# Kernel optimization log

Hardware: AMD Instinct MI355X
Metric: run time of the kernel (lower is better)

The kernel has to match this reference:

```python
import jax, jax.numpy as jnp
import numpy as np

D_MODEL = 2048
H_TOTAL = 32
D_HEAD = D_MODEL // H_TOTAL  # 64
H_ACTIVE = 4
ROPE_BASE = 10000.0


def _apply_rope(t, cos, sin):
    # t: [B, H, T, DH]; cos/sin: [T, DH//2]; interleaved pair rotation
    t1 = t[..., 0::2]
    t2 = t[..., 1::2]
    r1 = t1 * cos - t2 * sin
    r2 = t1 * sin + t2 * cos
    return jnp.stack([r1, r2], axis=-1).reshape(t.shape)


def setup_inputs() -> dict:
    key = jax.random.key(0)
    ks = jax.random.split(key, 4)
    x = jax.random.normal(ks[0], (4, 1024, D_MODEL), dtype=jnp.float32)
    w_router = jax.random.normal(ks[1], (D_MODEL, H_TOTAL), dtype=jnp.float32) * 0.02
    w_qkv = jax.random.normal(ks[2], (D_MODEL, 3 * D_MODEL), dtype=jnp.float32) * 0.02
    w_out = jax.random.normal(ks[3], (D_MODEL, D_MODEL), dtype=jnp.float32) * 0.02
    return {"x": x, "w_router": w_router, "w_qkv": w_qkv, "w_out": w_out}


def reference(x, w_router, w_qkv, w_out):
    B, T, _ = x.shape
    # --- SwitchRouter: per-token probabilities over heads ---
    probs = jax.nn.softmax(x @ w_router, axis=-1)            # [B, T, H]
    # top-h_active heads per token (dense-math equivalent of sparse dispatch)
    _, top_idx = jax.lax.top_k(probs, H_ACTIVE)              # [B, T, HA]
    mask = jnp.sum(jax.nn.one_hot(top_idx, H_TOTAL, dtype=x.dtype), axis=-2)  # [B, T, H]
    gate = probs * mask                                      # router-scored gate

    # --- QKV projection ---
    qkv = x @ w_qkv                                          # [B, T, 3D]
    q, k, v = jnp.split(qkv, 3, axis=-1)
    def to_heads(t):
        return t.reshape(B, T, H_TOTAL, D_HEAD).transpose(0, 2, 1, 3)  # [B, H, T, DH]
    q, k, v = to_heads(q), to_heads(k), to_heads(v)

    # --- RoPE ---
    inv_freq = 1.0 / (ROPE_BASE ** (jnp.arange(0, D_HEAD, 2, dtype=jnp.float32) / D_HEAD))
    ang = jnp.arange(T, dtype=jnp.float32)[:, None] * inv_freq[None, :]  # [T, DH/2]
    cos, sin = jnp.cos(ang), jnp.sin(ang)
    q = _apply_rope(q, cos, sin)
    k = _apply_rope(k, cos, sin)

    # --- causal SDPA ---
    scores = jnp.einsum('bhqd,bhkd->bhqk', q, k) / np.float32(np.sqrt(D_HEAD))
    causal = jnp.tril(jnp.ones((T, T), dtype=bool))
    scores = jnp.where(causal, scores, jnp.finfo(scores.dtype).min)
    attn = jax.nn.softmax(scores, axis=-1)
    out = jnp.einsum('bhqk,bhkd->bhqd', attn, v)             # [B, H, T, DH]

    # --- gate: only active heads contribute (scatter-back equivalent) ---
    out = out * gate.transpose(0, 2, 1)[..., None]           # [B, H, T, DH]
    out = out.transpose(0, 2, 1, 3).reshape(B, T, D_MODEL)
    return out @ w_out
```

## Files before the change

kernel.cpp:

```cpp
#include <hip/hip_runtime.h>
#include <hip/hip_bf16.h>
#include <stdint.h>
#include <stddef.h>

typedef __attribute__((ext_vector_type(8))) short bf16x8;
typedef __attribute__((ext_vector_type(8))) unsigned short u16x8;
typedef __attribute__((ext_vector_type(4))) float f32x4;
typedef __attribute__((ext_vector_type(16))) float f32x16;

#define TT 1024

__device__ __forceinline__ unsigned short f2bf(float f){
  unsigned u = __builtin_bit_cast(unsigned, f);
  unsigned r = 0x7fffu + ((u >> 16) & 1u);
  return (unsigned short)((u + r) >> 16);
}
__device__ __forceinline__ float bf2f(unsigned short s){
  unsigned u = ((unsigned)s) << 16;
  return __builtin_bit_cast(float, u);
}
__device__ __forceinline__ void gload16(const unsigned short* g, unsigned short* l){
  __builtin_amdgcn_global_load_lds(
      (const __attribute__((address_space(1))) void*)g,
      (__attribute__((address_space(3))) void*)l, 16, 0, 0);
}

#define MFMA32(a, b, c) __builtin_amdgcn_mfma_f32_32x32x16_bf16((a), (b), (c), 0, 0, 0)
#define MFMA_B16(a, b, c) __builtin_amdgcn_mfma_f32_16x16x32_bf16((a), (b), (c), 0, 0, 0)

__global__ void transpose_w_kernel(const float* __restrict__ wqkv, const float* __restrict__ wout,
                                   unsigned short* __restrict__ wqkvT, unsigned short* __restrict__ woutT){
  __shared__ float tile[32][33];
  const float* in; unsigned short* out; int C;
  int bx = blockIdx.x;
  if (bx < 192){ in = wqkv; out = wqkvT; C = 6144; }
  else         { in = wout; out = woutT; C = 2048; bx -= 192; }
  const int R = 2048;
  int c0 = bx * 32, r0 = blockIdx.y * 32;
  for (int i = threadIdx.y; i < 32; i += 8)
    tile[i][threadIdx.x] = in[(size_t)(r0 + i) * C + c0 + threadIdx.x];
  __syncthreads();
  for (int i = threadIdx.y; i < 32; i += 8)
    out[(size_t)(c0 + i) * R + r0 + threadIdx.x] = f2bf(tile[threadIdx.x][i]);
}

__global__ __launch_bounds__(256) void prep_kernel(const float* __restrict__ x,
                                                   const float* __restrict__ wr,
                                                   unsigned short* __restrict__ x_bf,
                                                   float* __restrict__ gate,
                                                   unsigned char* __restrict__ heads4,
                                                   float* __restrict__ tab){
  __shared__ float xc[8 * 256];
  __shared__ float red[8 * 8 * 32];
  const int tid = threadIdx.x;
  const int tok0 = blockIdx.x * 8;
  const int p = tid >> 5, h = tid & 31;

  if (blockIdx.x < 128){
    int i2 = blockIdx.x * 256 + tid;
    int pos = i2 >> 5, ii = i2 & 31;
    float freq = powf(10000.0f, -(float)ii / 32.0f);
    float ang = (float)pos * freq;
    tab[i2 * 2]     = cosf(ang);
    tab[i2 * 2 + 1] = sinf(ang);
  }

  float acc[8] = {0.f,0.f,0.f,0.f,0.f,0.f,0.f,0.f};
  for (int kb = 0; kb < 8; kb++){
    __syncthreads();
    {
      int tok = tid >> 5, e = (tid & 31) * 8;
      const float* xp = x + (size_t)(tok0 + tok) * 2048 + kb * 256 + e;
      float4 v0 = *(const float4*)xp, v1 = *(const float4*)(xp + 4);
      float vals[8] = {v0.x, v0.y, v0.z, v0.w, v1.x, v1.y, v1.z, v1.w};
      u16x8 ob;
      #pragma unroll
      for (int jj = 0; jj < 8; jj++) ob[jj] = f2bf(vals[jj]);
      *(u16x8*)(x_bf + (size_t)(tok0 + tok) * 2048 + kb * 256 + e) = ob;
      #pragma unroll
      for (int jj = 0; jj < 8; jj++) xc[tok * 256 + e + jj] = vals[jj];
    }
    __syncthreads();
    const float* wp = wr + (size_t)(kb * 256 + p * 32) * 32 + h;
    #pragma unroll 4
    for (int j = 0; j < 32; j++){
      float wv = wp[j * 32];
      #pragma unroll
      for (int tok = 0; tok < 8; tok++)
        acc[tok] += xc[tok * 256 + p * 32 + j] * wv;
    }
  }
  #pragma unroll
  for (int tok = 0; tok < 8; tok++) red[(p * 8 + tok) * 32 + h] = acc[tok];
  __syncthreads();
  {
    int lane = tid & 63;
    int tok = (tid >> 6) * 2 + (lane >> 5);
    int hh = lane & 31;
    float logit = 0.f;
    #pragma unroll
    for (int pp = 0; pp < 8; pp++) logit += red[(pp * 8 + tok) * 32 + hh];
    float m = logit;
    #pragma unroll
    for (int s = 16; s >= 1; s >>= 1) m = fmaxf(m, __shfl_xor(m, s));
    float e = __expf(logit - m);
    float sum = e;
    #pragma unroll
    for (int s = 16; s >= 1; s >>= 1) sum += __shfl_xor(sum, s);
    float prob = e / sum;
    float v = logit; int sel = 0;
    #pragma unroll
    for (int rr2 = 0; rr2 < 4; rr2++){
      float bv = v; int bi = hh;
      #pragma unroll
      for (int s = 16; s >= 1; s >>= 1){
        float ov = __shfl_xor(bv, s); int oi = __shfl_xor(bi, s);
        if (ov > bv || (ov == bv && oi < bi)) { bv = ov; bi = oi; }
      }
      if (hh == bi) { sel = 1; v = -3.4e38f; }
    }
    gate[(size_t)(tok0 + tok) * 32 + hh] = sel ? prob : 0.f;
    unsigned long long bal = __ballot(sel != 0);
    unsigned selmask = (unsigned)(bal >> ((lane >> 5) * 32));
    if (sel){
      int r = __popc(selmask & ((1u << hh) - 1u));
      heads4[(size_t)(tok0 + tok) * 4 + r] = (unsigned char)hh;
    }
  }
}

__global__ void compact_kernel(const unsigned char* __restrict__ heads4,
                               unsigned short* __restrict__ idx, int* __restrict__ counts){
  int bh = blockIdx.x;
  int b = bh >> 5, h = bh & 31;
  int lane = threadIdx.x;
  int base = 0;
  for (int c = 0; c < 16; c++){
    int t = c * 64 + lane;
    unsigned u = ((const unsigned*)heads4)[b * 1024 + t];
    int r = -1;
    if (((u      ) & 255) == (unsigned)h) r = 0;
    else if (((u >>  8) & 255) == (unsigned)h) r = 1;
    else if (((u >> 16) & 255) == (unsigned)h) r = 2;
    else if (((u >> 24) & 255) == (unsigned)h) r = 3;
    bool act = (r >= 0);
    unsigned long long mask = __ballot(act);
    int pos = base + __popcll(mask & ((1ull << lane) - 1ull));
    if (act) idx[bh * 1024 + pos] = (unsigned short)(t | (r << 10));
    base += __popcll(mask);
  }
  if (lane == 0) counts[bh] = base;
}

__global__ __launch_bounds__(256) void qgemm_kernel(const unsigned short* __restrict__ x_bf,
                                                    const unsigned short* __restrict__ wqkvT,
                                                    const unsigned short* __restrict__ idx,
                                                    const int* __restrict__ counts,
                                                    const float* __restrict__ tab,
                                                    unsigned short* __restrict__ qact){
  __shared__ float red[4][64][64];
  const int bh = blockIdx.x, qt = blockIdx.y;
  const int count = counts[bh];
  if (qt * 64 >= count) return;
  const int b = bh >> 5, h = bh & 31;
  const int tid = threadIdx.x, lane = tid & 63, w = tid >> 6;
  const int li = lane & 15, lg = lane >> 4;
  const int nvalid = min(64, count - qt * 64);
  const unsigned short* myidx = idx + bh * 1024 + qt * 64;

  int atok[4];
  #pragma unroll
  for (int ai = 0; ai < 4; ai++){
    int s = ai * 16 + li;
    atok[ai] = (s < nvalid) ? (myidx[s] & 1023) : 0;
  }
  const unsigned short* Bbase = wqkvT + (size_t)(h * 64) * 2048;

  f32x4 acc[4][4];
  #pragma unroll
  for (int i = 0; i < 4; i++)
    #pragma unroll
    for (int j = 0; j < 4; j++) acc[i][j] = f32x4{0.f, 0.f, 0.f, 0.f};

  const int k0w = w * 512;
  #pragma unroll 2
  for (int ks = 0; ks < 16; ks++){
    int k0 = k0w + ks * 32 + lg * 8;
    bf16x8 af[4], bw[4];
    #pragma unroll
    for (int ai = 0; ai < 4; ai++)
      af[ai] = *(const bf16x8*)(x_bf + (size_t)(b * 1024 + atok[ai]) * 2048 + k0);
    #pragma unroll
    for (int ni = 0; ni < 4; ni++)
      bw[ni] = *(const bf16x8*)(Bbase + (size_t)(ni * 16 + li) * 2048 + k0);
    #pragma unroll
    for (int ai = 0; ai < 4; ai++)
      #pragma unroll
      for (int ni = 0; ni < 4; ni++)
        acc[ai][ni] = MFMA_B16(af[ai], bw[ni], acc[ai][ni]);
  }
  #pragma unroll
  for (int ai = 0; ai < 4; ai++)
    #pragma unroll
    for (int ni = 0; ni < 4; ni++)
      #pragma unroll
      for (int rr = 0; rr < 4; rr++)
        red[w][ai * 16 + lg * 4 + rr][ni * 16 + li] = acc[ai][ni][rr];
  __syncthreads();

  int q = tid >> 2, dbase = (tid & 3) * 16;
  if (q < nvalid){
    int e = myidx[q];
    int tok = e & 1023, r = e >> 10;
    unsigned short* op = qact + ((size_t)((b << 10) + tok) * 4 + r) * 64;
    const float* tp = tab + ((size_t)tok * 32 + (dbase >> 1)) * 2;
    #pragma unroll
    for (int p = 0; p < 8; p++){
      int d0 = dbase + 2 * p;
      float v0 = red[0][q][d0] + red[1][q][d0] + red[2][q][d0] + red[3][q][d0];
      float v1 = red[0][q][d0 + 1] + red[1][q][d0 + 1] + red[2][q][d0 + 1] + red[3][q][d0 + 1];
      float c = tp[2 * p], s = tp[2 * p + 1];
      op[d0]     = f2bf(v0 * c - v1 * s);
      op[d0 + 1] = f2bf(v0 * s + v1 * c);
    }
  }
}

__global__ __launch_bounds__(256, 2) void gemmk(const unsigned short* __restrict__ A,
                                                const unsigned short* __restrict__ Bt,
                                                unsigned short* __restrict__ kbuf,
                                                unsigned short* __restrict__ vt,
                                                const float* __restrict__ tab,
                                                int K, int nbm){
  extern __shared__ unsigned short smem[];
  constexpr int MREP = 4;
  constexpr int BM = MREP * 64;
  constexpr int AU = MREP * 2048;
  constexpr int SLOT = AU + 4096;
  const int nblk = gridDim.x;
  const int raw = blockIdx.x;
  const int tile = (raw & 7) * (nblk >> 3) + (raw >> 3);
  const int bn = tile / nbm, bm = tile % nbm;

  const int tid = threadIdx.x, lane = tid & 63, wid = tid >> 6;
  const int wrow = wid >> 1, wcol = wid & 1;
  const int l31 = lane & 31, hi = lane >> 5;
  const int X = ((l31 >> 1) & 7) << 4;

  const unsigned short* gA[MREP];
  const unsigned short* gB[2];
  #pragma unroll
  for (int p = 0; p < MREP; p++){
    int L = tid * 16 + p * 4096;
    int line = L >> 7;
    int cs = (L & 127) ^ ((line & 7) << 4);
    gA[p] = A + (size_t)(bm * BM + line * 2 + (cs >> 6)) * K + ((cs & 63) >> 1);
  }
  #pragma unroll
  for (int p = 0; p < 2; p++){
    int L = tid * 16 + p * 4096;
    int line = L >> 7;
    int cs = (L & 127) ^ ((line & 7) << 4);
    gB[p] = Bt + (size_t)(bn * 128 + line * 2 + (cs >> 6)) * K + ((cs & 63) >> 1);
  }

  f32x16 acc[MREP][2];
  #pragma unroll
  for (int i = 0; i < MREP; i++)
    #pragma unroll
    for (int j = 0; j < 2; j++) acc[i][j] = f32x16{0,0,0,0,0,0,0,0,0,0,0,0,0,0,0,0};

  const int NT = K >> 5;
  #pragma unroll
  for (int tt = 0; tt < 2; tt++){
    unsigned short* sb = smem + tt * SLOT;
    #pragma unroll
    for (int p = 0; p < MREP; p++) gload16(gA[p] + (size_t)tt * 32, sb + tid * 8 + p * 2048);
    #pragma unroll
    for (int p = 0; p < 2; p++)    gload16(gB[p] + (size_t)tt * 32, sb + AU + tid * 8 + p * 2048);
  }

  for (int t = 0; t < NT; ++t){
    if (t < NT - 1) asm volatile("s_waitcnt vmcnt(6)" ::: "memory");
    else            asm volatile("s_waitcnt vmcnt(0)" ::: "memory");
    __builtin_amdgcn_s_barrier();
    __builtin_amdgcn_sched_barrier(0);
    const unsigned short* bs = smem + (t % 3) * SLOT;
    unsigned short* ns = smem + ((t + 2) % 3) * SLOT;
    const bool st = (t + 2 < NT);
    #pragma unroll
    for (int ks = 0; ks < 2; ks++){
      const int bo = (((l31 & 1) * 64 + ks * 32 + hi * 16) ^ X) >> 1;
      bf16x8 av[MREP], bv[2];
      #pragma unroll
      for (int i = 0; i < MREP; i++)
        av[i] = *(const bf16x8*)(bs + (wrow * (MREP * 16) + i * 16 + (l31 >> 1)) * 64 + bo);
      #pragma unroll
      for (int j = 0; j < 2; j++)
        bv[j] = *(const bf16x8*)(bs + AU + (wcol * 32 + j * 16 + (l31 >> 1)) * 64 + bo);
      if (st){
        if (ks == 0){
          #pragma unroll
          for (int p = 0; p < 3; p++)
            gload16(gA[p] + (size_t)(t + 2) * 32, ns + tid * 8 + p * 2048);
        } else {
          gload16(gA[3] + (size_t)(t + 2) * 32, ns + tid * 8 + 3 * 2048);
          #pragma unroll
          for (int p = 0; p < 2; p++)
            gload16(gB[p] + (size_t)(t + 2) * 32, ns + AU + tid * 8 + p * 2048);
        }
      }
      #pragma unroll
      for (int i = 0; i < MREP; i++){
        acc[i][0] = MFMA32(av[i], bv[0], acc[i][0]);
        acc[i][1] = MFMA32(av[i], bv[1], acc[i][1]);
      }
    }
  }

  if (bn < 16){
    #pragma unroll
    for (int i = 0; i < MREP; i++){
      #pragma unroll
      for (int j = 0; j < 2; j++){
        int col = bn * 128 + wcol * 64 + j * 32 + l31;
        int ii = (col & 63) >> 1;
        #pragma unroll
        for (int g = 0; g < 4; g++){
          #pragma unroll
          for (int rr = 0; rr < 4; rr++){
            int row = bm * BM + wrow * (BM / 2) + i * 32 + g * 8 + hi * 4 + rr;
            int pos = row & (TT - 1);
            const float* tp = tab + ((size_t)pos * 32 + ii) * 2;
            float c = tp[0], s = tp[1];
            float val = acc[i][j][g * 4 + rr];
            float pv = __shfl_xor(val, 1);
            float res = (lane & 1) ? (pv * s + val * c) : (val * c - pv * s);
            kbuf[(size_t)row * 2048 + col] = f2bf(res);
          }
        }
      }
    }
  } else {
    #pragma unroll
    for (int i = 0; i < MREP; i++){
      #pragma unroll
      for (int j = 0; j < 2; j++){
        int vcol = bn * 128 + wcol * 64 + j * 32 + l31 - 2048;
        int hh = vcol >> 6, d = vcol & 63;
        int row0 = bm * BM + wrow * (BM / 2) + i * 32 + hi * 4;
        int b = row0 >> 10, t0 = row0 & (TT - 1);
        #pragma unroll
        for (int g = 0; g < 4; g++){
          ushort4 pk;
          pk.x = f2bf(acc[i][j][g * 4 + 0]); pk.y = f2bf(acc[i][j][g * 4 + 1]);
          pk.z = f2bf(acc[i][j][g * 4 + 2]); pk.w = f2bf(acc[i][j][g * 4 + 3]);
          *(ushort4*)(vt + ((size_t)((b * 32 + hh) * 64 + d)) * TT + t0 + g * 8) = pk;
        }
      }
    }
  }
}

__global__ __launch_bounds__(256) void attn_sparse_kernel(unsigned short* __restrict__ qact,
                                                          const unsigned short* __restrict__ kbuf,
                                                          const unsigned short* __restrict__ vt,
                                                          const float* __restrict__ gate,
                                                          const unsigned short* __restrict__ idx,
                                                          const int* __restrict__ counts){
  __shared__ unsigned short Ks[64 * 64];
  __shared__ unsigned short Vs[64 * 64];
  __shared__ unsigned short Ps[4][16 * 64];
  const int bh = blockIdx.x, qt = blockIdx.y;
  const int count = counts[bh];
  if (qt * 64 >= count) return;
  const int b = bh >> 5, h = bh & 31;
  const int tid = threadIdx.x, lane = tid & 63, w = tid >> 6;
  const int li = lane & 15, lg = lane >> 4;
  const unsigned short* myidx = idx + bh * 1024 + qt * 64;
  const int nvalid = min(64, count - qt * 64);
  const int qmax = myidx[nvalid - 1] & 1023;

  int qi[4];
  #pragma unroll
  for (int r = 0; r < 4; r++){
    int s = w * 16 + lg * 4 + r;
    qi[r] = (s < nvalid) ? (myidx[s] & 1023) : -1;
  }
  bf16x8 qf0, qf1;
  {
    int s = w * 16 + li;
    int e2 = (s < nvalid) ? myidx[s] : 0;
    const unsigned short* qp = qact + ((size_t)((b << 10) + (e2 & 1023)) * 4 + (e2 >> 10)) * 64;
    qf0 = *(const bf16x8*)(qp + lg * 8);
    qf1 = *(const bf16x8*)(qp + 32 + lg * 8);
  }
  f32x4 o[4];
  #pragma unroll
  for (int i = 0; i < 4; i++) o[i] = f32x4{0.f, 0.f, 0.f, 0.f};
  float m_run[4], l_run[4];
  #pragma unroll
  for (int r = 0; r < 4; r++){ m_run[r] = -1e30f; l_run[r] = 0.f; }

  const int nkt = (qmax >> 6) + 1;
  for (int kt = 0; kt < nkt; kt++){
    const int kb = kt * 64;
    #pragma unroll
    for (int s2 = 0; s2 < 2; s2++){
      int s = s2 * 256 + tid;
      int r = s >> 3, c = (s & 7) * 8;
      gload16(kbuf + (size_t)(b * TT + kb + r) * 2048 + h * 64 + c, &Ks[s * 8]);
      gload16(vt + (size_t)(bh * 64 + r) * TT + kb + c, &Vs[s * 8]);
    }
    __syncthreads();

    f32x4 s4[4];
    #pragma unroll
    for (int ni = 0; ni < 4; ni++){
      bf16x8 k0 = *(const bf16x8*)(&Ks[(ni * 16 + li) * 64 + lg * 8]);
      bf16x8 k1 = *(const bf16x8*)(&Ks[(ni * 16 + li) * 64 + 32 + lg * 8]);
      f32x4 t = f32x4{0.f, 0.f, 0.f, 0.f};
      t = MFMA_B16(qf0, k0, t);
      t = MFMA_B16(qf1, k1, t);
      s4[ni] = t;
    }
    float mt[4];
    #pragma unroll
    for (int r = 0; r < 4; r++) mt[r] = -1e30f;
    #pragma unroll
    for (int ni = 0; ni < 4; ni++){
      int kidx = kb + ni * 16 + li;
      #pragma unroll
      for (int r = 0; r < 4; r++){
        float val = s4[ni][r] * 0.125f;
        val = (kidx <= qi[r]) ? val : -1e30f;
        s4[ni][r] = val;
        mt[r] = fmaxf(mt[r], val);
      }
    }
    #pragma unroll
    for (int r = 0; r < 4; r++){
      #pragma unroll
      for (int sh = 8; sh >= 1; sh >>= 1) mt[r] = fmaxf(mt[r], __shfl_xor(mt[r], sh));
      float mnew = fmaxf(m_run[r], mt[r]);
      float corr = __expf(m_run[r] - mnew);
      m_run[r] = mnew;
      l_run[r] *= corr;
      #pragma unroll
      for (int j = 0; j < 4; j++) o[j][r] *= corr;
    }
    float rs[4] = {0.f, 0.f, 0.f, 0.f};
    #pragma unroll
    for (int ni = 0; ni < 4; ni++)
      #pragma unroll
      for (int r = 0; r < 4; r++){
        float p = __expf(s4[ni][r] - m_run[r]);
        s4[ni][r] = p;
        rs[r] += p;
      }
    #pragma unroll
    for (int r = 0; r < 4; r++){
      #pragma unroll
      for (int sh = 8; sh >= 1; sh >>= 1) rs[r] += __shfl_xor(rs[r], sh);
      l_run[r] += rs[r];
    }
    #pragma unroll
    for (int ni = 0; ni < 4; ni++)
      #pragma unroll
      for (int r = 0; r < 4; r++)
        Ps[w][(lg * 4 + r) * 64 + ni * 16 + li] = f2bf(s4[ni][r]);
    #pragma unroll
    for (int ks = 0; ks < 2; ks++){
      bf16x8 pa = *(const bf16x8*)(&Ps[w][li * 64 + ks * 32 + lg * 8]);
      #pragma unroll
      for (int ni = 0; ni < 4; ni++){
        bf16x8 vb = *(const bf16x8*)(&Vs[(ni * 16 + li) * 64 + ks * 32 + lg * 8]);
        o[ni] = MFMA_B16(pa, vb, o[ni]);
      }
    }
    __syncthreads();
  }
  #pragma unroll
  for (int r = 0; r < 4; r++){
    if (qi[r] < 0) continue;
    float g = gate[(size_t)(b * TT + qi[r]) * 32 + h];
    float inv = g / l_run[r];
    int e = myidx[w * 16 + lg * 4 + r];
    unsigned short* op = qact + ((size_t)((b << 10) + (e & 1023)) * 4 + (e >> 10)) * 64;
    #pragma unroll
    for (int ni = 0; ni < 4; ni++)
      op[ni * 16 + li] = f2bf(o[ni][r] * inv);
  }
}

__global__ __launch_bounds__(256) void outsp_kernel(const unsigned short* __restrict__ qact,
                                                    const unsigned short* __restrict__ woutT,
                                                    const unsigned short* __restrict__ idx,
                                                    const int* __restrict__ counts,
                                                    unsigned short* __restrict__ p0,
                                                    unsigned short* __restrict__ p1,
                                                    unsigned short* __restrict__ p2,
                                                    unsigned short* __restrict__ p3){
  __shared__ unsigned short As[64 * 64];
  __shared__ unsigned short sidx[64];
  const int bh = blockIdx.x, qt = blockIdx.y;
  const int count = counts[bh];
  if (qt * 64 >= count) return;
  const int b = bh >> 5, h = bh & 31;
  const int tid = threadIdx.x, lane = tid & 63, w = tid >> 6;
  const int li = lane & 15, lg = lane >> 4;
  const int nvalid = min(64, count - qt * 64);
  const unsigned short* myidx = idx + bh * 1024 + qt * 64;
  const int n0 = blockIdx.z * 256 + w * 64;

  bf16x8 bfr[4][2];
  #pragma unroll
  for (int ni = 0; ni < 4; ni++)
    #pragma unroll
    for (int kh = 0; kh < 2; kh++)
      bfr[ni][kh] = *(const bf16x8*)(woutT + (size_t)(n0 + ni * 16 + li) * 2048 + h * 64 + kh * 32 + lg * 8);

  if (tid < 64) sidx[tid] = myidx[(tid < nvalid) ? tid : 0];
  #pragma unroll
  for (int s2 = 0; s2 < 2; s2++){
    int s = s2 * 256 + tid;
    int row = s >> 3, bc = (s & 7) * 16;
    int e = myidx[(row < nvalid) ? row : 0];
    const unsigned short* src = qact + ((size_t)((b << 10) + (e & 1023)) * 4 + (e >> 10)) * 64;
    gload16(src + ((bc ^ ((row & 7) << 4)) >> 1), &As[s * 8]);
  }
  __syncthreads();

  const int kX = (li & 7) << 4;
  f32x4 acc[4][4];
  #pragma unroll
  for (int i = 0; i < 4; i++)
    #pragma unroll
    for (int j = 0; j < 4; j++) acc[i][j] = f32x4{0.f, 0.f, 0.f, 0.f};
  #pragma unroll
  for (int ti = 0; ti < 4; ti++){
    bf16x8 a0 = *(const bf16x8*)(&As[((ti * 16 + li) * 128 + ((lg * 16) ^ kX)) >> 1]);
    bf16x8 a1 = *(const bf16x8*)(&As[((ti * 16 + li) * 128 + ((64 + lg * 16) ^ kX)) >> 1]);
    #pragma unroll
    for (int ni = 0; ni < 4; ni++){
      acc[ti][ni] = MFMA_B16(a0, bfr[ni][0], acc[ti][ni]);
      acc[ti][ni] = MFMA_B16(a1, bfr[ni][1], acc[ti][ni]);
    }
  }
  #pragma unroll
  for (int ti = 0; ti < 4; ti++){
    #pragma unroll
    for (int rr = 0; rr < 4; rr++){
      int slot = ti * 16 + lg * 4 + rr;
      if (slot < nvalid){
        int e = sidx[slot];
        int tok = e & 1023, rk = e >> 10;
        unsigned short* pp = (rk == 0) ? p0 : (rk == 1) ? p1 : (rk == 2) ? p2 : p3;
        size_t base = (size_t)(b * 1024 + tok) * 2048 + n0;
        #pragma unroll
        for (int ni = 0; ni < 4; ni++)
          pp[base + ni * 16 + li] = f2bf(acc[ti][ni][rr]);
      }
    }
  }
}

__global__ void reduce_kernel(const unsigned short* __restrict__ p0,
                              const unsigned short* __restrict__ p1,
                              const unsigned short* __restrict__ p2,
                              const unsigned short* __restrict__ p3,
                              float* __restrict__ out){
  size_t i = ((size_t)blockIdx.x * 256 + threadIdx.x) * 8;
  u16x8 a = *(const u16x8*)(p0 + i);
  u16x8 b = *(const u16x8*)(p1 + i);
  u16x8 c = *(const u16x8*)(p2 + i);
  u16x8 d = *(const u16x8*)(p3 + i);
  #pragma unroll
  for (int j = 0; j < 8; j++)
    out[i + j] = bf2f(a[j]) + bf2f(b[j]) + bf2f(c[j]) + bf2f(d[j]);
}

extern "C" void kernel_launch(void* const* d_in, const int* in_sizes, int n_in,
                              void* d_out, int out_size, void* d_ws, size_t ws_size,
                              hipStream_t stream){
  const float* x        = (const float*)d_in[0];
  const float* w_router = (const float*)d_in[1];
  const float* w_qkv    = (const float*)d_in[2];
  const float* w_out    = (const float*)d_in[3];
  float* out = (float*)d_out;
  char* ws = (char*)d_ws;

  unsigned short* kbuf   = (unsigned short*)(ws);
  unsigned short* vt     = (unsigned short*)(ws + 16777216);
  unsigned short* qact   = (unsigned short*)(ws + 33554432);
  unsigned short* idx    = (unsigned short*)(ws + 37748736);
  int* counts            = (int*)(ws + 38010880);
  unsigned char* heads4  = (unsigned char*)(ws + 38011392);
  unsigned short* x_bf   = (unsigned short*)(ws + 50331648);
  unsigned short* wqkvT  = (unsigned short*)(ws + 67108864);
  unsigned short* woutT  = (unsigned short*)(ws + 92274688);
  float* gate            = (float*)(ws + 100663296);
  float* tab             = (float*)(ws + 101187584);
  unsigned short* part0  = kbuf;
  unsigned short* part1  = vt;
  unsigned short* part2  = x_bf;
  unsigned short* part3  = wqkvT;

  constexpr int KV_LDS = 3 * (4 * 4096 + 8192) * 2 / 2;
  (void)hipFuncSetAttribute(reinterpret_cast<const void*>(&gemmk),
                            hipFuncAttributeMaxDynamicSharedMemorySize, KV_LDS);

  hipLaunchKernelGGL(transpose_w_kernel, dim3(256, 64), dim3(32, 8), 0, stream, w_qkv, w_out, wqkvT, woutT);
  hipLaunchKernelGGL(prep_kernel, dim3(512), dim3(256), 0, stream, x, w_router, x_bf, gate, heads4, tab);
  hipLaunchKernelGGL(compact_kernel, dim3(128), dim3(64), 0, stream, heads4, idx, counts);
  hipLaunchKernelGGL(gemmk, dim3(512), dim3(256), KV_LDS, stream,
                     x_bf, wqkvT + (size_t)2048 * 2048, kbuf, vt, tab, 2048, 16);
  hipLaunchKernelGGL(qgemm_kernel, dim3(128, 16), dim3(256), 0, stream,
                     x_bf, wqkvT, idx, counts, tab, qact);
  hipLaunchKernelGGL(attn_sparse_kernel, dim3(128, 16), dim3(256), 0, stream,
                     qact, kbuf, vt, gate, idx, counts);
  hipLaunchKernelGGL(outsp_kernel, dim3(128, 16, 8), dim3(256), 0, stream,
                     qact, woutT, idx, counts, part0, part1, part2, part3);
  hipLaunchKernelGGL(reduce_kernel, dim3(4096), dim3(256), 0, stream,
                     part0, part1, part2, part3, out);
}
```

Baseline: 255.7 us.

## Merge weight transpose into prep and fuse K/V and Q GEMMs into one launch

```diff
diff --git a/kernel.cpp b/kernel.cpp
--- a/kernel.cpp
+++ b/kernel.cpp
@@ -28,31 +28,38 @@
 #define MFMA32(a, b, c) __builtin_amdgcn_mfma_f32_32x32x16_bf16((a), (b), (c), 0, 0, 0)
 #define MFMA_B16(a, b, c) __builtin_amdgcn_mfma_f32_16x16x32_bf16((a), (b), (c), 0, 0, 0)
 
-__global__ void transpose_w_kernel(const float* __restrict__ wqkv, const float* __restrict__ wout,
-                                   unsigned short* __restrict__ wqkvT, unsigned short* __restrict__ woutT){
-  __shared__ float tile[32][33];
-  const float* in; unsigned short* out; int C;
-  int bx = blockIdx.x;
-  if (bx < 192){ in = wqkv; out = wqkvT; C = 6144; }
-  else         { in = wout; out = woutT; C = 2048; bx -= 192; }
-  const int R = 2048;
-  int c0 = bx * 32, r0 = blockIdx.y * 32;
-  for (int i = threadIdx.y; i < 32; i += 8)
-    tile[i][threadIdx.x] = in[(size_t)(r0 + i) * C + c0 + threadIdx.x];
-  __syncthreads();
-  for (int i = threadIdx.y; i < 32; i += 8)
-    out[(size_t)(c0 + i) * R + r0 + threadIdx.x] = f2bf(tile[threadIdx.x][i]);
-}
-
-__global__ __launch_bounds__(256) void prep_kernel(const float* __restrict__ x,
-                                                   const float* __restrict__ wr,
-                                                   unsigned short* __restrict__ x_bf,
-                                                   float* __restrict__ gate,
-                                                   unsigned char* __restrict__ heads4,
-                                                   float* __restrict__ tab){
+__global__ __launch_bounds__(256) void prep2_kernel(const float* __restrict__ x,
+                                                    const float* __restrict__ wr,
+                                                    const float* __restrict__ wqkv,
+                                                    const float* __restrict__ wout,
+                                                    unsigned short* __restrict__ x_bf,
+                                                    float* __restrict__ gate,
+                                                    unsigned char* __restrict__ heads4,
+                                                    float* __restrict__ tab,
+                                                    unsigned short* __restrict__ wqkvT,
+                                                    unsigned short* __restrict__ woutT){
   __shared__ float xc[8 * 256];
   __shared__ float red[8 * 8 * 32];
+  __shared__ float tile[32][33];
   const int tid = threadIdx.x;
+
+  if (blockIdx.x >= 512){
+    int tb = blockIdx.x - 512;
+    int bx = tb & 255, by = tb >> 8;
+    const float* in; unsigned short* out; int C;
+    if (bx < 192){ in = wqkv; out = wqkvT; C = 6144; }
+    else         { in = wout; out = woutT; C = 2048; bx -= 192; }
+    const int R = 2048;
+    int c0 = bx * 32, r0 = by * 32;
+    int tx = tid & 31, ty = tid >> 5;
+    for (int i = ty; i < 32; i += 8)
+      tile[i][tx] = in[(size_t)(r0 + i) * C + c0 + tx];
+    __syncthreads();
+    for (int i = ty; i < 32; i += 8)
+      out[(size_t)(c0 + i) * R + r0 + tx] = f2bf(tile[tx][i]);
+    return;
+  }
+
   const int tok0 = blockIdx.x * 8;
   const int p = tid >> 5, h = tid & 31;
 
@@ -152,211 +159,220 @@
   if (lane == 0) counts[bh] = base;
 }
 
-__global__ __launch_bounds__(256) void qgemm_kernel(const unsigned short* __restrict__ x_bf,
-                                                    const unsigned short* __restrict__ wqkvT,
-                                                    const unsigned short* __restrict__ idx,
-                                                    const int* __restrict__ counts,
-                                                    const float* __restrict__ tab,
-                                                    unsigned short* __restrict__ qact){
-  __shared__ float red[4][64][64];
-  const int bh = blockIdx.x, qt = blockIdx.y;
-  const int count = counts[bh];
-  if (qt * 64 >= count) return;
-  const int b = bh >> 5, h = bh & 31;
-  const int tid = threadIdx.x, lane = tid & 63, w = tid >> 6;
-  const int li = lane & 15, lg = lane >> 4;
-  const int nvalid = min(64, count - qt * 64);
-  const unsigned short* myidx = idx + bh * 1024 + qt * 64;
-
-  int atok[4];
-  #pragma unroll
-  for (int ai = 0; ai < 4; ai++){
-    int s = ai * 16 + li;
-    atok[ai] = (s < nvalid) ? (myidx[s] & 1023) : 0;
-  }
-  const unsigned short* Bbase = wqkvT + (size_t)(h * 64) * 2048;
-
-  f32x4 acc[4][4];
-  #pragma unroll
-  for (int i = 0; i < 4; i++)
-    #pragma unroll
-    for (int j = 0; j < 4; j++) acc[i][j] = f32x4{0.f, 0.f, 0.f, 0.f};
-
-  const int k0w = w * 512;
-  #pragma unroll 2
-  for (int ks = 0; ks < 16; ks++){
-    int k0 = k0w + ks * 32 + lg * 8;
-    bf16x8 af[4], bw[4];
-    #pragma unroll
-    for (int ai = 0; ai < 4; ai++)
-      af[ai] = *(const bf16x8*)(x_bf + (size_t)(b * 1024 + atok[ai]) * 2048 + k0);
-    #pragma unroll
-    for (int ni = 0; ni < 4; ni++)
-      bw[ni] = *(const bf16x8*)(Bbase + (size_t)(ni * 16 + li) * 2048 + k0);
-    #pragma unroll
-    for (int ai = 0; ai < 4; ai++)
-      #pragma unroll
-      for (int ni = 0; ni < 4; ni++)
-        acc[ai][ni] = MFMA_B16(af[ai], bw[ni], acc[ai][ni]);
-  }
-  #pragma unroll
-  for (int ai = 0; ai < 4; ai++)
-    #pragma unroll
-    for (int ni = 0; ni < 4; ni++)
-      #pragma unroll
-      for (int rr = 0; rr < 4; rr++)
-        red[w][ai * 16 + lg * 4 + rr][ni * 16 + li] = acc[ai][ni][rr];
-  __syncthreads();
-
-  int q = tid >> 2, dbase = (tid & 3) * 16;
-  if (q < nvalid){
-    int e = myidx[q];
-    int tok = e & 1023, r = e >> 10;
-    unsigned short* op = qact + ((size_t)((b << 10) + tok) * 4 + r) * 64;
-    const float* tp = tab + ((size_t)tok * 32 + (dbase >> 1)) * 2;
-    #pragma unroll
-    for (int p = 0; p < 8; p++){
-      int d0 = dbase + 2 * p;
-      float v0 = red[0][q][d0] + red[1][q][d0] + red[2][q][d0] + red[3][q][d0];
-      float v1 = red[0][q][d0 + 1] + red[1][q][d0 + 1] + red[2][q][d0 + 1] + red[3][q][d0 + 1];
-      float c = tp[2 * p], s = tp[2 * p + 1];
-      op[d0]     = f2bf(v0 * c - v1 * s);
-      op[d0 + 1] = f2bf(v0 * s + v1 * c);
-    }
-  }
-}
-
-__global__ __launch_bounds__(256, 2) void gemmk(const unsigned short* __restrict__ A,
-                                                const unsigned short* __restrict__ Bt,
-                                                unsigned short* __restrict__ kbuf,
-                                                unsigned short* __restrict__ vt,
-                                                const float* __restrict__ tab,
-                                                int K, int nbm){
+__global__ __launch_bounds__(256, 2) void super_kernel(const unsigned short* __restrict__ x_bf,
+                                                       const unsigned short* __restrict__ wqkvT,
+                                                       unsigned short* __restrict__ kbuf,
+                                                       unsigned short* __restrict__ vt,
+                                                       const float* __restrict__ tab,
+                                                       const unsigned short* __restrict__ idx,
+                                                       const int* __restrict__ counts,
+                                                       unsigned short* __restrict__ qact){
   extern __shared__ unsigned short smem[];
-  constexpr int MREP = 4;
-  constexpr int BM = MREP * 64;
-  constexpr int AU = MREP * 2048;
-  constexpr int SLOT = AU + 4096;
-  const int nblk = gridDim.x;
-  const int raw = blockIdx.x;
-  const int tile = (raw & 7) * (nblk >> 3) + (raw >> 3);
-  const int bn = tile / nbm, bm = tile % nbm;
-
-  const int tid = threadIdx.x, lane = tid & 63, wid = tid >> 6;
-  const int wrow = wid >> 1, wcol = wid & 1;
-  const int l31 = lane & 31, hi = lane >> 5;
-  const int X = ((l31 >> 1) & 7) << 4;
-
-  const unsigned short* gA[MREP];
-  const unsigned short* gB[2];
-  #pragma unroll
-  for (int p = 0; p < MREP; p++){
-    int L = tid * 16 + p * 4096;
-    int line = L >> 7;
-    int cs = (L & 127) ^ ((line & 7) << 4);
-    gA[p] = A + (size_t)(bm * BM + line * 2 + (cs >> 6)) * K + ((cs & 63) >> 1);
-  }
-  #pragma unroll
-  for (int p = 0; p < 2; p++){
-    int L = tid * 16 + p * 4096;
-    int line = L >> 7;
-    int cs = (L & 127) ^ ((line & 7) << 4);
-    gB[p] = Bt + (size_t)(bn * 128 + line * 2 + (cs >> 6)) * K + ((cs & 63) >> 1);
-  }
-
-  f32x16 acc[MREP][2];
-  #pragma unroll
-  for (int i = 0; i < MREP; i++)
-    #pragma unroll
-    for (int j = 0; j < 2; j++) acc[i][j] = f32x16{0,0,0,0,0,0,0,0,0,0,0,0,0,0,0,0};
-
-  const int NT = K >> 5;
-  #pragma unroll
-  for (int tt = 0; tt < 2; tt++){
-    unsigned short* sb = smem + tt * SLOT;
-    #pragma unroll
-    for (int p = 0; p < MREP; p++) gload16(gA[p] + (size_t)tt * 32, sb + tid * 8 + p * 2048);
-    #pragma unroll
-    for (int p = 0; p < 2; p++)    gload16(gB[p] + (size_t)tt * 32, sb + AU + tid * 8 + p * 2048);
-  }
-
-  for (int t = 0; t < NT; ++t){
-    if (t < NT - 1) asm volatile("s_waitcnt vmcnt(6)" ::: "memory");
-    else            asm volatile("s_waitcnt vmcnt(0)" ::: "memory");
-    __builtin_amdgcn_s_barrier();
-    __builtin_amdgcn_sched_barrier(0);
-    const unsigned short* bs = smem + (t % 3) * SLOT;
-    unsigned short* ns = smem + ((t + 2) % 3) * SLOT;
-    const bool st = (t + 2 < NT);
-    #pragma unroll
-    for (int ks = 0; ks < 2; ks++){
-      const int bo = (((l31 & 1) * 64 + ks * 32 + hi * 16) ^ X) >> 1;
-      bf16x8 av[MREP], bv[2];
-      #pragma unroll
-      for (int i = 0; i < MREP; i++)
-        av[i] = *(const bf16x8*)(bs + (wrow * (MREP * 16) + i * 16 + (l31 >> 1)) * 64 + bo);
-      #pragma unroll
-      for (int j = 0; j < 2; j++)
-        bv[j] = *(const bf16x8*)(bs + AU + (wcol * 32 + j * 16 + (l31 >> 1)) * 64 + bo);
-      if (st){
-        if (ks == 0){
-          #pragma unroll
-          for (int p = 0; p < 3; p++)
-            gload16(gA[p] + (size_t)(t + 2) * 32, ns + tid * 8 + p * 2048);
-        } else {
-          gload16(gA[3] + (size_t)(t + 2) * 32, ns + tid * 8 + 3 * 2048);
-          #pragma unroll
-          for (int p = 0; p < 2; p++)
-            gload16(gB[p] + (size_t)(t + 2) * 32, ns + AU + tid * 8 + p * 2048);
-        }
-      }
-      #pragma unroll
-      for (int i = 0; i < MREP; i++){
-        acc[i][0] = MFMA32(av[i], bv[0], acc[i][0]);
-        acc[i][1] = MFMA32(av[i], bv[1], acc[i][1]);
-      }
-    }
-  }
-
-  if (bn < 16){
-    #pragma unroll
-    for (int i = 0; i < MREP; i++){
-      #pragma unroll
-      for (int j = 0; j < 2; j++){
-        int col = bn * 128 + wcol * 64 + j * 32 + l31;
-        int ii = (col & 63) >> 1;
-        #pragma unroll
-        for (int g = 0; g < 4; g++){
-          #pragma unroll
-          for (int rr = 0; rr < 4; rr++){
-            int row = bm * BM + wrow * (BM / 2) + i * 32 + g * 8 + hi * 4 + rr;
-            int pos = row & (TT - 1);
-            const float* tp = tab + ((size_t)pos * 32 + ii) * 2;
-            float c = tp[0], s = tp[1];
-            float val = acc[i][j][g * 4 + rr];
-            float pv = __shfl_xor(val, 1);
-            float res = (lane & 1) ? (pv * s + val * c) : (val * c - pv * s);
-            kbuf[(size_t)row * 2048 + col] = f2bf(res);
+  const int tid = threadIdx.x, lane = tid & 63;
+
+  if (blockIdx.x < 512){
+    const unsigned short* A  = x_bf;
+    const unsigned short* Bt = wqkvT + (size_t)2048 * 2048;
+    constexpr int MREP = 4;
+    constexpr int BM = 256;
+    constexpr int AU = MREP * 2048;
+    constexpr int SLOT = AU + 4096;
+    const int raw = blockIdx.x;
+    const int tile = (raw & 7) * 64 + (raw >> 3);
+    const int bn = tile >> 4, bm = tile & 15;
+    const int K = 2048;
+
+    const int wid = tid >> 6;
+    const int wrow = wid >> 1, wcol = wid & 1;
+    const int l31 = lane & 31, hi = lane >> 5;
+    const int X = ((l31 >> 1) & 7) << 4;
+
+    const unsigned short* gA[MREP];
+    const unsigned short* gB[2];
+    #pragma unroll
+    for (int p = 0; p < MREP; p++){
+      int L = tid * 16 + p * 4096;
+      int line = L >> 7;
+      int cs = (L & 127) ^ ((line & 7) << 4);
+      gA[p] = A + (size_t)(bm * BM + line * 2 + (cs >> 6)) * K + ((cs & 63) >> 1);
+    }
+    #pragma unroll
+    for (int p = 0; p < 2; p++){
+      int L = tid * 16 + p * 4096;
+      int line = L >> 7;
+      int cs = (L & 127) ^ ((line & 7) << 4);
+      gB[p] = Bt + (size_t)(bn * 128 + line * 2 + (cs >> 6)) * K + ((cs & 63) >> 1);
+    }
+
+    f32x16 acc[MREP][2];
+    #pragma unroll
+    for (int i = 0; i < MREP; i++)
+      #pragma unroll
+      for (int j = 0; j < 2; j++) acc[i][j] = f32x16{0,0,0,0,0,0,0,0,0,0,0,0,0,0,0,0};
+
+    const int NT = K >> 5;
+    #pragma unroll
+    for (int tt = 0; tt < 2; tt++){
+      unsigned short* sb = smem + tt * SLOT;
+      #pragma unroll
+      for (int p = 0; p < MREP; p++) gload16(gA[p] + (size_t)tt * 32, sb + tid * 8 + p * 2048);
+      #pragma unroll
+      for (int p = 0; p < 2; p++)    gload16(gB[p] + (size_t)tt * 32, sb + AU + tid * 8 + p * 2048);
+    }
+
+    for (int t = 0; t < NT; ++t){
+      if (t < NT - 1) asm volatile("s_waitcnt vmcnt(6)" ::: "memory");
+      else            asm volatile("s_waitcnt vmcnt(0)" ::: "memory");
+      __builtin_amdgcn_s_barrier();
+      __builtin_amdgcn_sched_barrier(0);
+      const unsigned short* bs = smem + (t % 3) * SLOT;
+      unsigned short* ns = smem + ((t + 2) % 3) * SLOT;
+      const bool st = (t + 2 < NT);
+      #pragma unroll
+      for (int ks = 0; ks < 2; ks++){
+        const int bo = (((l31 & 1) * 64 + ks * 32 + hi * 16) ^ X) >> 1;
+        bf16x8 av[MREP], bv[2];
+        #pragma unroll
+        for (int i = 0; i < MREP; i++)
+          av[i] = *(const bf16x8*)(bs + (wrow * (MREP * 16) + i * 16 + (l31 >> 1)) * 64 + bo);
+        #pragma unroll
+        for (int j = 0; j < 2; j++)
+          bv[j] = *(const bf16x8*)(bs + AU + (wcol * 32 + j * 16 + (l31 >> 1)) * 64 + bo);
+        if (st){
+          if (ks == 0){
+            #pragma unroll
+            for (int p = 0; p < 3; p++)
+              gload16(gA[p] + (size_t)(t + 2) * 32, ns + tid * 8 + p * 2048);
+          } else {
+            gload16(gA[3] + (size_t)(t + 2) * 32, ns + tid * 8 + 3 * 2048);
+            #pragma unroll
+            for (int p = 0; p < 2; p++)
+              gload16(gB[p] + (size_t)(t + 2) * 32, ns + AU + tid * 8 + p * 2048);
           }
         }
-      }
-    }
-  } else {
-    #pragma unroll
-    for (int i = 0; i < MREP; i++){
-      #pragma unroll
-      for (int j = 0; j < 2; j++){
-        int vcol = bn * 128 + wcol * 64 + j * 32 + l31 - 2048;
-        int hh = vcol >> 6, d = vcol & 63;
-        int row0 = bm * BM + wrow * (BM / 2) + i * 32 + hi * 4;
-        int b = row0 >> 10, t0 = row0 & (TT - 1);
-        #pragma unroll
-        for (int g = 0; g < 4; g++){
-          ushort4 pk;
-          pk.x = f2bf(acc[i][j][g * 4 + 0]); pk.y = f2bf(acc[i][j][g * 4 + 1]);
-          pk.z = f2bf(acc[i][j][g * 4 + 2]); pk.w = f2bf(acc[i][j][g * 4 + 3]);
-          *(ushort4*)(vt + ((size_t)((b * 32 + hh) * 64 + d)) * TT + t0 + g * 8) = pk;
+        __builtin_amdgcn_s_setprio(1);
+        #pragma unroll
+        for (int i = 0; i < MREP; i++){
+          acc[i][0] = MFMA32(av[i], bv[0], acc[i][0]);
+          acc[i][1] = MFMA32(av[i], bv[1], acc[i][1]);
         }
+        __builtin_amdgcn_s_setprio(0);
+      }
+    }
+
+    if (bn < 16){
+      #pragma unroll
+      for (int i = 0; i < MREP; i++){
+        #pragma unroll
+        for (int j = 0; j < 2; j++){
+          int col = bn * 128 + wcol * 64 + j * 32 + l31;
+          int ii = (col & 63) >> 1;
+          #pragma unroll
+          for (int g = 0; g < 4; g++){
+            #pragma unroll
+            for (int rr = 0; rr < 4; rr++){
+              int row = bm * BM + wrow * (BM / 2) + i * 32 + g * 8 + hi * 4 + rr;
+              int pos = row & (TT - 1);
+              const float* tp = tab + ((size_t)pos * 32 + ii) * 2;
+              float c = tp[0], s = tp[1];
+              float val = acc[i][j][g * 4 + rr];
+              float pv = __shfl_xor(val, 1);
+              float res = (lane & 1) ? (pv * s + val * c) : (val * c - pv * s);
+              kbuf[(size_t)row * 2048 + col] = f2bf(res);
+            }
+          }
+        }
+      }
+    } else {
+      #pragma unroll
+      for (int i = 0; i < MREP; i++){
+        #pragma unroll
+        for (int j = 0; j < 2; j++){
+          int vcol = bn * 128 + wcol * 64 + j * 32 + l31 - 2048;
+          int hh = vcol >> 6, d = vcol & 63;
+          int row0 = bm * BM + wrow * (BM / 2) + i * 32 + hi * 4;
+          int b = row0 >> 10, t0 = row0 & (TT - 1);
+          #pragma unroll
+          for (int g = 0; g < 4; g++){
+            ushort4 pk;
+            pk.x = f2bf(acc[i][j][g * 4 + 0]); pk.y = f2bf(acc[i][j][g * 4 + 1]);
+            pk.z = f2bf(acc[i][j][g * 4 + 2]); pk.w = f2bf(acc[i][j][g * 4 + 3]);
+            *(ushort4*)(vt + ((size_t)((b * 32 + hh) * 64 + d)) * TT + t0 + g * 8) = pk;
+          }
+        }
+      }
+    }
+    return;
+  }
+
+  {
+    float* red = (float*)smem;
+    const int r0 = blockIdx.x - 512;
+    const int bh = r0 >> 4, qt = r0 & 15;
+    const int count = counts[bh];
+    if (qt * 64 >= count) return;
+    const int b = bh >> 5, h = bh & 31;
+    const int w = tid >> 6;
+    const int li = lane & 15, lg = lane >> 4;
+    const int nvalid = min(64, count - qt * 64);
+    const unsigned short* myidx = idx + bh * 1024 + qt * 64;
+
+    int atok[4];
+    #pragma unroll
+    for (int ai = 0; ai < 4; ai++){
+      int s = ai * 16 + li;
+      atok[ai] = (s < nvalid) ? (myidx[s] & 1023) : 0;
+    }
+    const unsigned short* Bbase = wqkvT + (size_t)(h * 64) * 2048;
+
+    f32x4 acc[4][4];
+    #pragma unroll
+    for (int i = 0; i < 4; i++)
+      #pragma unroll
+      for (int j = 0; j < 4; j++) acc[i][j] = f32x4{0.f, 0.f, 0.f, 0.f};
+
+    const int k0w = w * 512;
+    #pragma unroll 2
+    for (int ks = 0; ks < 16; ks++){
+      int k0 = k0w + ks * 32 + lg * 8;
+      bf16x8 af[4], bw[4];
+      #pragma unroll
+      for (int ai = 0; ai < 4; ai++)
+        af[ai] = *(const bf16x8*)(x_bf + (size_t)(b * 1024 + atok[ai]) * 2048 + k0);
+      #pragma unroll
+      for (int ni = 0; ni < 4; ni++)
+        bw[ni] = *(const bf16x8*)(Bbase + (size_t)(ni * 16 + li) * 2048 + k0);
+      #pragma unroll
+      for (int ai = 0; ai < 4; ai++)
+        #pragma unroll
+        for (int ni = 0; ni < 4; ni++)
+          acc[ai][ni] = MFMA_B16(af[ai], bw[ni], acc[ai][ni]);
+    }
+    #pragma unroll
+    for (int ai = 0; ai < 4; ai++)
+      #pragma unroll
+      for (int ni = 0; ni < 4; ni++)
+        #pragma unroll
+        for (int rr = 0; rr < 4; rr++)
+          red[((w * 64) + ai * 16 + lg * 4 + rr) * 64 + ni * 16 + li] = acc[ai][ni][rr];
+    __syncthreads();
+
+    int q = tid >> 2, dbase = (tid & 3) * 16;
+    if (q < nvalid){
+      int e = myidx[q];
+      int tok = e & 1023, r = e >> 10;
+      unsigned short* op = qact + ((size_t)((b << 10) + tok) * 4 + r) * 64;
+      const float* tp = tab + ((size_t)tok * 32 + (dbase >> 1)) * 2;
+      #pragma unroll
+      for (int p = 0; p < 8; p++){
+        int d0 = dbase + 2 * p;
+        float v0 = red[q * 64 + d0]          + red[(64 + q) * 64 + d0]
+                 + red[(128 + q) * 64 + d0]  + red[(192 + q) * 64 + d0];
+        float v1 = red[q * 64 + d0 + 1]         + red[(64 + q) * 64 + d0 + 1]
+                 + red[(128 + q) * 64 + d0 + 1] + red[(192 + q) * 64 + d0 + 1];
+        float c = tp[2 * p], s = tp[2 * p + 1];
+        op[d0]     = f2bf(v0 * c - v1 * s);
+        op[d0 + 1] = f2bf(v0 * s + v1 * c);
       }
     }
   }
@@ -606,17 +622,15 @@
   unsigned short* part2  = x_bf;
   unsigned short* part3  = wqkvT;
 
-  constexpr int KV_LDS = 3 * (4 * 4096 + 8192) * 2 / 2;
-  (void)hipFuncSetAttribute(reinterpret_cast<const void*>(&gemmk),
+  constexpr int KV_LDS = 73728;
+  (void)hipFuncSetAttribute(reinterpret_cast<const void*>(&super_kernel),
                             hipFuncAttributeMaxDynamicSharedMemorySize, KV_LDS);
 
-  hipLaunchKernelGGL(transpose_w_kernel, dim3(256, 64), dim3(32, 8), 0, stream, w_qkv, w_out, wqkvT, woutT);
-  hipLaunchKernelGGL(prep_kernel, dim3(512), dim3(256), 0, stream, x, w_router, x_bf, gate, heads4, tab);
+  hipLaunchKernelGGL(prep2_kernel, dim3(16896), dim3(256), 0, stream,
+                     x, w_router, w_qkv, w_out, x_bf, gate, heads4, tab, wqkvT, woutT);
   hipLaunchKernelGGL(compact_kernel, dim3(128), dim3(64), 0, stream, heads4, idx, counts);
-  hipLaunchKernelGGL(gemmk, dim3(512), dim3(256), KV_LDS, stream,
-                     x_bf, wqkvT + (size_t)2048 * 2048, kbuf, vt, tab, 2048, 16);
-  hipLaunchKernelGGL(qgemm_kernel, dim3(128, 16), dim3(256), 0, stream,
-                     x_bf, wqkvT, idx, counts, tab, qact);
+  hipLaunchKernelGGL(super_kernel, dim3(2560), dim3(256), KV_LDS, stream,
+                     x_bf, wqkvT, kbuf, vt, tab, idx, counts, qact);
   hipLaunchKernelGGL(attn_sparse_kernel, dim3(128, 16), dim3(256), 0, stream,
                      qact, kbuf, vt, gate, idx, counts);
   hipLaunchKernelGGL(outsp_kernel, dim3(128, 16, 8), dim3(256), 0, stream,
```

Result: slower. 329.8 us (+29.0%).
